# Optimization experiments

Measured on AMD Instinct MI355X. Metric: run time of the kernel, lower is better.

The kernel has to match this reference:

```python
import jax, jax.numpy as jnp
import numpy as np

B, N, E, H = 2, 2048, 768, 12
HD = E // H  # 64


def setup_inputs() -> dict:
    key = jax.random.key(0)
    k1, k2, k3 = jax.random.split(key, 3)
    x = jax.random.normal(k1, (B, N, E), dtype=jnp.float32)
    # PyTorch nn.Linear default init scale ~ 1/sqrt(fan_in); keep scores sane
    w_qkv = jax.random.normal(k2, (E, 3 * E), dtype=jnp.float32) * (E ** -0.5)
    b_qkv = jnp.zeros((3 * E,), dtype=jnp.float32)
    w_out = jax.random.normal(k3, (E, E), dtype=jnp.float32) * (E ** -0.5)
    b_out = jnp.zeros((E,), dtype=jnp.float32)
    return {"x": x, "w_qkv": w_qkv, "b_qkv": b_qkv, "w_out": w_out, "b_out": b_out}


def reference(x, w_qkv, b_qkv, w_out, b_out):
    # fused QKV projection: [B,N,E] @ [E,3E] -> [B,N,3E]
    qkv = x @ w_qkv + b_qkv
    qkv = qkv.reshape(B, N, 3, H, HD)
    qkv = jnp.transpose(qkv, (2, 0, 3, 1, 4))  # [3,B,H,N,HD]
    q, k, v = qkv[0], qkv[1], qkv[2]
    scale = HD ** -0.5
    # scores: [B,H,N,N]
    scores = jnp.einsum('bhnd,bhmd->bhnm', q, k) * scale
    attn_probs = jax.nn.softmax(scores, axis=-1)
    # dropout is identity (p=0 / eval mode)
    out = jnp.einsum('bhnm,bhmd->bhnd', attn_probs, v)  # [B,H,N,HD]
    out = jnp.transpose(out, (0, 2, 1, 3)).reshape(B, N, E)
    out = out @ w_out + b_out
    return out, attn_probs
```

## Files before the change

### kernel.cpp

```cpp
#include <hip/hip_runtime.h>


typedef __bf16 bf16x8 __attribute__((ext_vector_type(8)));
typedef float  f32x4  __attribute__((ext_vector_type(4)));

__device__ __forceinline__ unsigned short f2bf(float f) {
  union { float f; unsigned int u; } v; v.f = f;
  unsigned int r = v.u + 0x7FFFu + ((v.u >> 16) & 1u);
  return (unsigned short)(r >> 16);
}

template<bool A_BF16, bool OUT_BF16>
__global__ __launch_bounds__(256) void gemm_bias_kernel(
    const void* __restrict__ Av, const float* __restrict__ B,
    const float* __restrict__ bias, void* __restrict__ Cv,
    int M, int N, int K)
{
  __shared__ __align__(16) unsigned short Alds[128][40];
  __shared__ __align__(16) unsigned short Btl [128][40];

  const int tid  = threadIdx.x;
  const int lane = tid & 63;
  const int w    = tid >> 6;
  const int wr   = w >> 1, wc = w & 1;
  const int l16  = lane & 15, lg = lane >> 4;
  const int tn   = blockIdx.x, tm = blockIdx.y;

  f32x4 acc[4][4];
#pragma unroll
  for (int m = 0; m < 4; ++m)
#pragma unroll
    for (int n = 0; n < 4; ++n) acc[m][n] = (f32x4){0.f, 0.f, 0.f, 0.f};

  const int nkt = K >> 5;
  for (int kt = 0; kt < nkt; ++kt) {
    if (A_BF16) {
      const unsigned short* A = (const unsigned short*)Av;
#pragma unroll
      for (int it = 0; it < 2; ++it) {
        int id = tid + it * 256;
        int r = id >> 2, c8 = id & 3;
        *(uint4*)&Alds[r][c8 * 8] =
            *(const uint4*)(A + (size_t)(tm * 128 + r) * K + kt * 32 + c8 * 8);
      }
    } else {
      const float* A = (const float*)Av;
#pragma unroll
      for (int it = 0; it < 4; ++it) {
        int id = tid + it * 256;
        int r = id >> 3, c4 = id & 7;
        const float4 v = *(const float4*)(A + (size_t)(tm * 128 + r) * K + kt * 32 + c4 * 4);
        ushort4 u;
        u.x = f2bf(v.x); u.y = f2bf(v.y); u.z = f2bf(v.z); u.w = f2bf(v.w);
        *(ushort4*)&Alds[r][c4 * 4] = u;
      }
    }
#pragma unroll
    for (int it = 0; it < 4; ++it) {
      int id = tid + it * 256;
      int k = id >> 5, c4 = id & 31;
      const float4 v = *(const float4*)(B + (size_t)(kt * 32 + k) * N + tn * 128 + c4 * 4);
      Btl[c4 * 4 + 0][k] = f2bf(v.x);
      Btl[c4 * 4 + 1][k] = f2bf(v.y);
      Btl[c4 * 4 + 2][k] = f2bf(v.z);
      Btl[c4 * 4 + 3][k] = f2bf(v.w);
    }
    __syncthreads();

    bf16x8 af[4], bfr[4];
#pragma unroll
    for (int m = 0; m < 4; ++m)
      af[m] = *(const bf16x8*)&Alds[wr * 64 + m * 16 + l16][lg * 8];
#pragma unroll
    for (int n = 0; n < 4; ++n)
      bfr[n] = *(const bf16x8*)&Btl[wc * 64 + n * 16 + l16][lg * 8];
#pragma unroll
    for (int m = 0; m < 4; ++m)
#pragma unroll
      for (int n = 0; n < 4; ++n)
        acc[m][n] = __builtin_amdgcn_mfma_f32_16x16x32_bf16(af[m], bfr[n], acc[m][n], 0, 0, 0);
    __syncthreads();
  }

#pragma unroll
  for (int n = 0; n < 4; ++n) {
    const int col = tn * 128 + wc * 64 + n * 16 + l16;
    const float bv = bias[col];
#pragma unroll
    for (int m = 0; m < 4; ++m) {
#pragma unroll
      for (int rr = 0; rr < 4; ++rr) {
        const int row = tm * 128 + wr * 64 + m * 16 + lg * 4 + rr;
        const float val = acc[m][n][rr] + bv;
        if (OUT_BF16) ((unsigned short*)Cv)[(size_t)row * N + col] = f2bf(val);
        else          ((float*)Cv)[(size_t)row * N + col] = val;
      }
    }
  }
}

__global__ __launch_bounds__(256) void attn_kernel(
    const unsigned short* __restrict__ qkv,
    float* __restrict__ probs,
    unsigned short* __restrict__ attn_out)
{
  __shared__ __align__(16) unsigned short Kl [64][72];
  __shared__ __align__(16) unsigned short VTl[64][72];
  __shared__ __align__(16) unsigned short Pl [64][72];

  const int bh = blockIdx.x, qt = blockIdx.y;
  const int b = bh / 12, h = bh % 12;
  const int tid = threadIdx.x;
  const int lane = tid & 63, w = tid >> 6;
  const int l16 = lane & 15, lg = lane >> 4;
  const float scale = 0.125f;

  const size_t qoff = ((size_t)b * 2048 + qt * 64 + w * 16 + l16) * 2304 + h * 64 + lg * 8;
  const bf16x8 qf0 = *(const bf16x8*)(qkv + qoff);
  const bf16x8 qf1 = *(const bf16x8*)(qkv + qoff + 32);

  float rs[4] = {0.f, 0.f, 0.f, 0.f};
  for (int kt = 0; kt < 32; ++kt) {
#pragma unroll
    for (int it = 0; it < 2; ++it) {
      int id = tid + it * 256;
      int p = id >> 3, c8 = id & 7;
      *(uint4*)&Kl[p][c8 * 8] =
          *(const uint4*)(qkv + ((size_t)b * 2048 + kt * 64 + p) * 2304 + 768 + h * 64 + c8 * 8);
    }
    __syncthreads();
#pragma unroll
    for (int n = 0; n < 4; ++n) {
      const bf16x8 kf0 = *(const bf16x8*)&Kl[n * 16 + l16][lg * 8];
      const bf16x8 kf1 = *(const bf16x8*)&Kl[n * 16 + l16][32 + lg * 8];
      f32x4 s = (f32x4){0.f, 0.f, 0.f, 0.f};
      s = __builtin_amdgcn_mfma_f32_16x16x32_bf16(qf0, kf0, s, 0, 0, 0);
      s = __builtin_amdgcn_mfma_f32_16x16x32_bf16(qf1, kf1, s, 0, 0, 0);
#pragma unroll
      for (int rr = 0; rr < 4; ++rr) rs[rr] += __expf(s[rr] * scale);
    }
    __syncthreads();
  }
#pragma unroll
  for (int rr = 0; rr < 4; ++rr) {
    rs[rr] += __shfl_xor(rs[rr], 1);
    rs[rr] += __shfl_xor(rs[rr], 2);
    rs[rr] += __shfl_xor(rs[rr], 4);
    rs[rr] += __shfl_xor(rs[rr], 8);
    rs[rr] = 1.0f / rs[rr];
  }

  f32x4 oacc[4];
#pragma unroll
  for (int n = 0; n < 4; ++n) oacc[n] = (f32x4){0.f, 0.f, 0.f, 0.f};

  for (int kt = 0; kt < 32; ++kt) {
#pragma unroll
    for (int it = 0; it < 2; ++it) {
      int id = tid + it * 256;
      int p = id >> 3, c8 = id & 7;
      const size_t base = ((size_t)b * 2048 + kt * 64 + p) * 2304 + h * 64 + c8 * 8;
      *(uint4*)&Kl[p][c8 * 8] = *(const uint4*)(qkv + base + 768);
      uint4 vv = *(const uint4*)(qkv + base + 1536);
      const unsigned short* vs = (const unsigned short*)&vv;
#pragma unroll
      for (int j = 0; j < 8; ++j) VTl[c8 * 8 + j][p] = vs[j];
    }
    __syncthreads();

#pragma unroll
    for (int n = 0; n < 4; ++n) {
      const bf16x8 kf0 = *(const bf16x8*)&Kl[n * 16 + l16][lg * 8];
      const bf16x8 kf1 = *(const bf16x8*)&Kl[n * 16 + l16][32 + lg * 8];
      f32x4 s = (f32x4){0.f, 0.f, 0.f, 0.f};
      s = __builtin_amdgcn_mfma_f32_16x16x32_bf16(qf0, kf0, s, 0, 0, 0);
      s = __builtin_amdgcn_mfma_f32_16x16x32_bf16(qf1, kf1, s, 0, 0, 0);
#pragma unroll
      for (int rr = 0; rr < 4; ++rr) {
        const float p = __expf(s[rr] * scale) * rs[rr];
        const int qr = qt * 64 + w * 16 + lg * 4 + rr;
        probs[((size_t)bh * 2048 + qr) * 2048 + (size_t)kt * 64 + n * 16 + l16] = p;
        Pl[w * 16 + lg * 4 + rr][n * 16 + l16] = f2bf(p);
      }
    }
    __syncthreads();

    const bf16x8 pa0 = *(const bf16x8*)&Pl[w * 16 + l16][lg * 8];
    const bf16x8 pa1 = *(const bf16x8*)&Pl[w * 16 + l16][32 + lg * 8];
#pragma unroll
    for (int n = 0; n < 4; ++n) {
      const bf16x8 vb0 = *(const bf16x8*)&VTl[n * 16 + l16][lg * 8];
      const bf16x8 vb1 = *(const bf16x8*)&VTl[n * 16 + l16][32 + lg * 8];
      oacc[n] = __builtin_amdgcn_mfma_f32_16x16x32_bf16(pa0, vb0, oacc[n], 0, 0, 0);
      oacc[n] = __builtin_amdgcn_mfma_f32_16x16x32_bf16(pa1, vb1, oacc[n], 0, 0, 0);
    }
    __syncthreads();
  }

#pragma unroll
  for (int n = 0; n < 4; ++n)
#pragma unroll
    for (int rr = 0; rr < 4; ++rr) {
      const int qr = qt * 64 + w * 16 + lg * 4 + rr;
      attn_out[((size_t)b * 2048 + qr) * 768 + h * 64 + n * 16 + l16] = f2bf(oacc[n][rr]);
    }
}

extern "C" void kernel_launch(void* const* d_in, const int* in_sizes, int n_in,
                              void* d_out, int out_size, void* d_ws, size_t ws_size,
                              hipStream_t stream) {
  const float* x     = (const float*)d_in[0];
  const float* w_qkv = (const float*)d_in[1];
  const float* b_qkv = (const float*)d_in[2];
  const float* w_out = (const float*)d_in[3];
  const float* b_out = (const float*)d_in[4];

  float* out   = (float*)d_out;
  float* probs = out + 3145728;

  unsigned short* qkv_ws  = (unsigned short*)d_ws;
  unsigned short* attn_ws = qkv_ws + (size_t)4096 * 2304;

  gemm_bias_kernel<false, true><<<dim3(18, 32), 256, 0, stream>>>(
      (const void*)x, w_qkv, b_qkv, (void*)qkv_ws, 4096, 2304, 768);

  attn_kernel<<<dim3(24, 32), 256, 0, stream>>>(qkv_ws, probs, attn_ws);

  gemm_bias_kernel<true, false><<<dim3(6, 32), 256, 0, stream>>>(
      (const void*)attn_ws, w_out, b_out, (void*)out, 4096, 768, 768);
}
```

Baseline: 634.5 us.

## Transpose score MFMA to vectorize probs stores and pack V transpose writes

Swaps the MFMA operand order so each lane holds four consecutive key columns of one query row. The probs write becomes a float4 store and the P tile write a packed uint2 store, and the row-sum reduction collapses to one scalar with two shuffles. The V transpose now loads two adjacent rows per thread and writes 32-bit pairs into a repadded LDS tile, which cuts LDS store count and bank conflicts. The aim is to reduce the cost of the 200MB probs write and the LDS traffic, at the price of different LDS padding and indexing.

```diff
diff --git a/kernel.cpp b/kernel.cpp
--- a/kernel.cpp
+++ b/kernel.cpp
@@ -105,66 +105,68 @@
     unsigned short* __restrict__ attn_out)
 {
   __shared__ __align__(16) unsigned short Kl [64][72];
-  __shared__ __align__(16) unsigned short VTl[64][72];
+  __shared__ __align__(16) unsigned short VTl[64][88];
   __shared__ __align__(16) unsigned short Pl [64][72];
 
   const int bh = blockIdx.x, qt = blockIdx.y;
   const int b = bh / 12, h = bh % 12;
-  const int tid = threadIdx.x;
+  const int tid  = threadIdx.x;
   const int lane = tid & 63, w = tid >> 6;
-  const int l16 = lane & 15, lg = lane >> 4;
-  const float scale = 0.125f;
+  const int l16  = lane & 15, lg = lane >> 4;
 
   const size_t qoff = ((size_t)b * 2048 + qt * 64 + w * 16 + l16) * 2304 + h * 64 + lg * 8;
   const bf16x8 qf0 = *(const bf16x8*)(qkv + qoff);
   const bf16x8 qf1 = *(const bf16x8*)(qkv + qoff + 32);
 
-  float rs[4] = {0.f, 0.f, 0.f, 0.f};
+  const int sp  = tid >> 3;
+  const int sc8 = tid & 7;
+  const int vp  = (tid & 31) * 2;
+  const int vc8 = tid >> 5;
+  const size_t kbase = (size_t)b * 2048 * 2304 + 768  + h * 64;
+  const size_t vbase = (size_t)b * 2048 * 2304 + 1536 + h * 64;
+
+  float rs = 0.f;
   for (int kt = 0; kt < 32; ++kt) {
-#pragma unroll
-    for (int it = 0; it < 2; ++it) {
-      int id = tid + it * 256;
-      int p = id >> 3, c8 = id & 7;
-      *(uint4*)&Kl[p][c8 * 8] =
-          *(const uint4*)(qkv + ((size_t)b * 2048 + kt * 64 + p) * 2304 + 768 + h * 64 + c8 * 8);
-    }
+    const size_t rb = kbase + (size_t)kt * 64 * 2304;
+    *(uint4*)&Kl[sp][sc8 * 8]      = *(const uint4*)(qkv + rb + (size_t)sp * 2304 + sc8 * 8);
+    *(uint4*)&Kl[sp + 32][sc8 * 8] = *(const uint4*)(qkv + rb + (size_t)(sp + 32) * 2304 + sc8 * 8);
     __syncthreads();
 #pragma unroll
     for (int n = 0; n < 4; ++n) {
       const bf16x8 kf0 = *(const bf16x8*)&Kl[n * 16 + l16][lg * 8];
       const bf16x8 kf1 = *(const bf16x8*)&Kl[n * 16 + l16][32 + lg * 8];
       f32x4 s = (f32x4){0.f, 0.f, 0.f, 0.f};
-      s = __builtin_amdgcn_mfma_f32_16x16x32_bf16(qf0, kf0, s, 0, 0, 0);
-      s = __builtin_amdgcn_mfma_f32_16x16x32_bf16(qf1, kf1, s, 0, 0, 0);
-#pragma unroll
-      for (int rr = 0; rr < 4; ++rr) rs[rr] += __expf(s[rr] * scale);
-    }
-    __syncthreads();
-  }
-#pragma unroll
-  for (int rr = 0; rr < 4; ++rr) {
-    rs[rr] += __shfl_xor(rs[rr], 1);
-    rs[rr] += __shfl_xor(rs[rr], 2);
-    rs[rr] += __shfl_xor(rs[rr], 4);
-    rs[rr] += __shfl_xor(rs[rr], 8);
-    rs[rr] = 1.0f / rs[rr];
-  }
+      s = __builtin_amdgcn_mfma_f32_16x16x32_bf16(kf0, qf0, s, 0, 0, 0);
+      s = __builtin_amdgcn_mfma_f32_16x16x32_bf16(kf1, qf1, s, 0, 0, 0);
+      rs += __expf(s[0] * 0.125f) + __expf(s[1] * 0.125f)
+          + __expf(s[2] * 0.125f) + __expf(s[3] * 0.125f);
+    }
+    __syncthreads();
+  }
+  rs += __shfl_xor(rs, 16);
+  rs += __shfl_xor(rs, 32);
+  const float rsi = 1.0f / rs;
 
   f32x4 oacc[4];
 #pragma unroll
   for (int n = 0; n < 4; ++n) oacc[n] = (f32x4){0.f, 0.f, 0.f, 0.f};
 
+  const size_t prow = ((size_t)bh * 2048 + qt * 64 + w * 16 + l16) * 2048;
+
   for (int kt = 0; kt < 32; ++kt) {
-#pragma unroll
-    for (int it = 0; it < 2; ++it) {
-      int id = tid + it * 256;
-      int p = id >> 3, c8 = id & 7;
-      const size_t base = ((size_t)b * 2048 + kt * 64 + p) * 2304 + h * 64 + c8 * 8;
-      *(uint4*)&Kl[p][c8 * 8] = *(const uint4*)(qkv + base + 768);
-      uint4 vv = *(const uint4*)(qkv + base + 1536);
-      const unsigned short* vs = (const unsigned short*)&vv;
-#pragma unroll
-      for (int j = 0; j < 8; ++j) VTl[c8 * 8 + j][p] = vs[j];
+    const size_t rbk = kbase + (size_t)kt * 64 * 2304;
+    const size_t rbv = vbase + (size_t)kt * 64 * 2304;
+    *(uint4*)&Kl[sp][sc8 * 8]      = *(const uint4*)(qkv + rbk + (size_t)sp * 2304 + sc8 * 8);
+    *(uint4*)&Kl[sp + 32][sc8 * 8] = *(const uint4*)(qkv + rbk + (size_t)(sp + 32) * 2304 + sc8 * 8);
+    {
+      uint4 v0 = *(const uint4*)(qkv + rbv + (size_t)vp * 2304 + vc8 * 8);
+      uint4 v1 = *(const uint4*)(qkv + rbv + (size_t)(vp + 1) * 2304 + vc8 * 8);
+      const unsigned short* a0 = (const unsigned short*)&v0;
+      const unsigned short* a1 = (const unsigned short*)&v1;
+#pragma unroll
+      for (int j = 0; j < 8; ++j)
+        *(unsigned int*)&VTl[vc8 * 8 + j][vp] =
+            (unsigned int)a0[j] | ((unsigned int)a1[j] << 16);
     }
     __syncthreads();
 
@@ -173,15 +175,17 @@
       const bf16x8 kf0 = *(const bf16x8*)&Kl[n * 16 + l16][lg * 8];
       const bf16x8 kf1 = *(const bf16x8*)&Kl[n * 16 + l16][32 + lg * 8];
       f32x4 s = (f32x4){0.f, 0.f, 0.f, 0.f};
-      s = __builtin_amdgcn_mfma_f32_16x16x32_bf16(qf0, kf0, s, 0, 0, 0);
-      s = __builtin_amdgcn_mfma_f32_16x16x32_bf16(qf1, kf1, s, 0, 0, 0);
-#pragma unroll
-      for (int rr = 0; rr < 4; ++rr) {
-        const float p = __expf(s[rr] * scale) * rs[rr];
-        const int qr = qt * 64 + w * 16 + lg * 4 + rr;
-        probs[((size_t)bh * 2048 + qr) * 2048 + (size_t)kt * 64 + n * 16 + l16] = p;
-        Pl[w * 16 + lg * 4 + rr][n * 16 + l16] = f2bf(p);
-      }
+      s = __builtin_amdgcn_mfma_f32_16x16x32_bf16(kf0, qf0, s, 0, 0, 0);
+      s = __builtin_amdgcn_mfma_f32_16x16x32_bf16(kf1, qf1, s, 0, 0, 0);
+      const float p0 = __expf(s[0] * 0.125f) * rsi;
+      const float p1 = __expf(s[1] * 0.125f) * rsi;
+      const float p2 = __expf(s[2] * 0.125f) * rsi;
+      const float p3 = __expf(s[3] * 0.125f) * rsi;
+      *(float4*)&probs[prow + kt * 64 + n * 16 + lg * 4] = (float4){p0, p1, p2, p3};
+      uint2 u;
+      u.x = (unsigned int)f2bf(p0) | ((unsigned int)f2bf(p1) << 16);
+      u.y = (unsigned int)f2bf(p2) | ((unsigned int)f2bf(p3) << 16);
+      *(uint2*)&Pl[w * 16 + l16][n * 16 + lg * 4] = u;
     }
     __syncthreads();
 
```

After: 633.3 us. Within noise of the previous version (-0.2%).
